# Optimization experiments

Measured on AMD Instinct MI355X. Metric: run time of the kernel, lower is better.

Reference implementation:

```python
import jax, jax.numpy as jnp
import numpy as np

E, C, F, K = 8, 768, 3072, 2  # NUM_EXPERTS, EMBED_DIM, FFN_DIM, TOP_K


def setup_inputs() -> dict:
    key = jax.random.key(0)
    k0, k1, k2, k3 = jax.random.split(key, 4)
    B, T = 8, 2048
    return {
        "x": jax.random.normal(k0, (B, T, C), jnp.float32),
        "router_w": jax.random.normal(k1, (E, C), jnp.float32) * 0.02,
        "w1": jax.random.normal(k2, (E, C, F), jnp.float32) * 0.02,
        "b1": jnp.zeros((E, F), jnp.float32),
        "w2": jax.random.normal(k3, (E, F, C), jnp.float32) * 0.02,
        "b2": jnp.zeros((E, C), jnp.float32),
    }


def reference(x, router_w, w1, b1, w2, b2):
    # Dropout is inference-mode identity (eval). GELU is torch's exact (erf) variant.
    B, T, Cc = x.shape
    flat = x.reshape(-1, Cc)                                   # [N, C]
    logits = flat @ router_w.T                                 # [N, E]
    probs = jax.nn.softmax(logits.astype(jnp.float32), axis=-1)
    top_w, top_i = jax.lax.top_k(probs, K)                     # [N, K]
    top_w = (top_w / top_w.sum(-1, keepdims=True)).astype(x.dtype)
    out = jnp.zeros_like(flat)
    for e in range(E):
        # per-token combine weight for expert e (0 if token not routed to e)
        w_e = jnp.sum(top_w * (top_i == e), axis=-1)[:, None]  # [N, 1]
        h = jax.nn.gelu(flat @ w1[e] + b1[e], approximate=False)  # [N, F]
        out = out + w_e * (h @ w2[e] + b2[e])
    return out.reshape(B, T, Cc)
```

## Files before the change

kernel.cpp:

```cpp
#include <hip/hip_runtime.h>
#include <hip/hip_bf16.h>

#define NTOK 16384
#define CDIM 768
#define FDIM 3072
#define NEXP 8
#define NSLOT 32768
#define HBLK 128
#define MAXTILES 263

typedef __attribute__((ext_vector_type(8))) short bf16x8;
typedef __attribute__((ext_vector_type(4))) float f32x4;

__device__ __forceinline__ unsigned short f2bf(float f) {
  unsigned int u = __float_as_uint(f);
  u += 0x7FFFu + ((u >> 16) & 1u);
  return (unsigned short)(u >> 16);
}
__device__ __forceinline__ float bf2f(unsigned short h) {
  return __uint_as_float((unsigned int)h << 16);
}

__device__ __forceinline__ void async16(const void* g, void* l) {
  __builtin_amdgcn_global_load_lds(
      (const __attribute__((address_space(1))) unsigned int*)g,
      (__attribute__((address_space(3))) unsigned int*)l, 16, 0, 0);
}

__global__ __launch_bounds__(256)
void k_transpose(const float* __restrict__ src, unsigned short* __restrict__ dst,
                 int R, int Cc)
{
  __shared__ float tle[32][33];
  int e = blockIdx.z;
  int c0 = blockIdx.x * 32, r0 = blockIdx.y * 32;
  int tx = threadIdx.x & 31, ty = threadIdx.x >> 5;
  const float* s = src + (size_t)e * R * Cc;
  unsigned short* d = dst + (size_t)e * R * Cc;
#pragma unroll
  for (int i = 0; i < 4; ++i)
    tle[ty + i * 8][tx] = s[(size_t)(r0 + ty + i * 8) * Cc + c0 + tx];
  __syncthreads();
#pragma unroll
  for (int i = 0; i < 4; ++i)
    d[(size_t)(c0 + ty + i * 8) * R + r0 + tx] = f2bf(tle[tx][ty + i * 8]);
}

__global__ __launch_bounds__(256)
void k_router(const float* __restrict__ x, const float* __restrict__ rw,
              int* __restrict__ tk_e, float* __restrict__ tk_w)
{
  __shared__ float srw[NEXP * CDIM];
  int tid = threadIdx.x;
#pragma unroll
  for (int i = 0; i < (NEXP * CDIM / 4) / 256; ++i)
    ((float4*)srw)[tid + i * 256] = ((const float4*)rw)[tid + i * 256];
  __syncthreads();
  int lane = tid & 63, wid = tid >> 6;
  int t = blockIdx.x * 4 + wid;
  float a[NEXP];
#pragma unroll
  for (int e = 0; e < NEXP; ++e) a[e] = 0.f;
  const float* xr = x + (size_t)t * CDIM;
#pragma unroll
  for (int c = 0; c < CDIM / 64; ++c) {
    float xv = xr[c * 64 + lane];
#pragma unroll
    for (int e = 0; e < NEXP; ++e) a[e] += xv * srw[e * CDIM + c * 64 + lane];
  }
#pragma unroll
  for (int e = 0; e < NEXP; ++e) {
#pragma unroll
    for (int off = 32; off; off >>= 1) a[e] += __shfl_xor(a[e], off);
  }
  if (lane == 0) {
    int i0 = 0; float l0 = a[0];
#pragma unroll
    for (int e = 1; e < NEXP; ++e) if (a[e] > l0) { l0 = a[e]; i0 = e; }
    int i1 = -1; float l1 = -1e30f;
#pragma unroll
    for (int e = 0; e < NEXP; ++e) if (e != i0 && a[e] > l1) { l1 = a[e]; i1 = e; }
    float w0 = 1.f / (1.f + expf(l1 - l0));
    tk_e[2 * t] = i0;     tk_e[2 * t + 1] = i1;
    tk_w[2 * t] = w0;     tk_w[2 * t + 1] = 1.f - w0;
  }
}

__global__ __launch_bounds__(256)
void k_hist(const int* __restrict__ tk_e, int* __restrict__ blockhist)
{
  __shared__ int h[NEXP];
  int tid = threadIdx.x;
  if (tid < NEXP) h[tid] = 0;
  __syncthreads();
  int e = tk_e[blockIdx.x * 256 + tid];
  atomicAdd(&h[e], 1);
  __syncthreads();
  if (tid < NEXP) blockhist[blockIdx.x * NEXP + tid] = h[tid];
}

__global__ __launch_bounds__(512)
void k_scan2(const int* __restrict__ blockhist, int* __restrict__ counts,
             int* __restrict__ offsets, int* __restrict__ tp,
             int* __restrict__ blockbase)
{
  __shared__ int ltot[NEXP];
  __shared__ int loff[NEXP + 1];
  int tid = threadIdx.x;
  int lane = tid & 63, e = tid >> 6;
  int o0 = blockhist[lane * NEXP + e];
  int o1 = blockhist[(64 + lane) * NEXP + e];
  int h0 = o0, h1 = o1;
#pragma unroll
  for (int d = 1; d < 64; d <<= 1) { int v = __shfl_up(h0, d); if (lane >= d) h0 += v; }
  int s0 = __shfl(h0, 63);
#pragma unroll
  for (int d = 1; d < 64; d <<= 1) { int v = __shfl_up(h1, d); if (lane >= d) h1 += v; }
  h1 += s0;
  if (lane == 63) ltot[e] = h1;
  __syncthreads();
  if (tid == 0) {
    loff[0] = 0;
    int tpv = 0; tp[0] = 0;
    for (int k = 0; k < NEXP; ++k) {
      loff[k + 1] = loff[k] + ltot[k];
      counts[k] = ltot[k];
      offsets[k] = loff[k];
      tpv += (ltot[k] + 127) / 128;
      tp[k + 1] = tpv;
    }
    offsets[NEXP] = loff[NEXP];
  }
  __syncthreads();
  int base = loff[e];
  blockbase[lane * NEXP + e]        = base + h0 - o0;
  blockbase[(64 + lane) * NEXP + e] = base + h1 - o1;
}

__global__ __launch_bounds__(256)
void k_assign_gather(const float* __restrict__ x, const int* __restrict__ tk_e,
                     const float* __restrict__ tk_w,
                     const int* __restrict__ blockbase,
                     int* __restrict__ tok2slot, float* __restrict__ slot_w,
                     unsigned short* __restrict__ Xg)
{
  __shared__ int eh[256];
  __shared__ int sslot[256];
  int b = blockIdx.x, tid = threadIdx.x;
  int pick = b * 256 + tid;
  int e = tk_e[pick];
  eh[tid] = e;
  __syncthreads();
  int rank = 0;
  for (int j = 0; j < tid; ++j) rank += (eh[j] == e);
  int slot = blockbase[b * NEXP + e] + rank;
  sslot[tid] = slot;
  tok2slot[pick] = slot;
  slot_w[slot] = tk_w[pick];
  __syncthreads();
  int lane = tid & 63, wid = tid >> 6;
  for (int p = wid * 64; p < wid * 64 + 64; ++p) {
    int token = (b * 256 + p) >> 1;
    int s = sslot[p];
    const float4* src = (const float4*)(x + (size_t)token * CDIM);
    ushort4* dst = (ushort4*)(Xg + (size_t)s * CDIM);
#pragma unroll
    for (int i = 0; i < 3; ++i) {
      float4 v = src[i * 64 + lane];
      ushort4 hh;
      hh.x = f2bf(v.x); hh.y = f2bf(v.y); hh.z = f2bf(v.z); hh.w = f2bf(v.w);
      dst[i * 64 + lane] = hh;
    }
  }
}

template <int EPI>
__device__ __forceinline__ void gemm_body(
    const unsigned short* __restrict__ A, int lda,
    const unsigned short* __restrict__ B, int ldb, long sB,
    int Ksteps,
    const int* __restrict__ counts, const int* __restrict__ offsets,
    const int* __restrict__ tp, int t0,
    const float* __restrict__ bias, int biasStride,
    unsigned short* __restrict__ Hout, int ldh,
    unsigned short* __restrict__ Yout, const float* __restrict__ slot_w,
    int gx, int nwg)
{
  __shared__ __align__(16) char lds[5 * 16384];

  int orig = blockIdx.y * gx + blockIdx.x;
  int q = nwg >> 3, r = nwg & 7;
  int xcd = orig & 7, j = orig >> 3;
  int wgid = (xcd < r ? xcd * (q + 1) : r * (q + 1) + (xcd - r) * q) + j;
  int bx = wgid % gx, byl = wgid / gx;
  int by = t0 + byl;

  if (by >= tp[NEXP]) return;
  int e = 0;
  while (by >= tp[e + 1]) ++e;
  int m0 = (by - tp[e]) * 128;
  int cnt = counts[e];
  int rowbase = offsets[e];
  int n0 = bx * 128;

  const unsigned short* Bexp = B + (long)e * sB + (long)n0 * ldb;
  const unsigned short* Aexp =
      (EPI == 0) ? A + (long)(rowbase + m0) * lda
                 : A + (long)(byl * 128) * lda;

  int tid = threadIdx.x;
  int lane = tid & 63, wid = tid >> 6;
  int wm = wid >> 1, wn = wid & 1;
  int ar = lane & 15, kg = lane >> 4;
  int kgs = (kg ^ ((ar >> 1) & 3)) << 4;

  int rA0 = tid >> 2;
  int cA0 = tid & 3;
  int ksw = (cA0 ^ ((rA0 >> 1) & 3)) << 3;
  const unsigned short* As0 = Aexp + (long)rA0 * lda + ksw;
  const unsigned short* As1 = Aexp + (long)(rA0 + 64) * lda + ksw;
  const unsigned short* Bs0 = Bexp + (long)rA0 * ldb + ksw;
  const unsigned short* Bs1 = Bexp + (long)(rA0 + 64) * ldb + ksw;

  f32x4 acc[4][4] = {};

  auto STAGE = [&](int t) {
    char* bb = lds + (t % 5) * 16384;
    int ko = t * 32;
    async16(As0 + ko, bb + wid * 1024);
    async16(As1 + ko, bb + 4096 + wid * 1024);
    async16(Bs0 + ko, bb + 8192 + wid * 1024);
    async16(Bs1 + ko, bb + 12288 + wid * 1024);
  };

  STAGE(0); STAGE(1); STAGE(2);

  for (int ks = 0; ks < Ksteps; ++ks) {
    if (ks + 3 < Ksteps) {
      STAGE(ks + 3);
      asm volatile("s_waitcnt vmcnt(12)" ::: "memory");
    } else if (ks + 2 < Ksteps) {
      asm volatile("s_waitcnt vmcnt(8)" ::: "memory");
    } else if (ks + 1 < Ksteps) {
      asm volatile("s_waitcnt vmcnt(4)" ::: "memory");
    } else {
      asm volatile("s_waitcnt vmcnt(0)" ::: "memory");
    }
    __builtin_amdgcn_s_barrier();
    asm volatile("" ::: "memory");

    const char* bb = lds + (ks % 5) * 16384;
    const char* bA = bb + (wm * 64 + ar) * 64 + kgs;
    const char* bB = bb + 8192 + (wn * 64 + ar) * 64 + kgs;
    bf16x8 af[4], bfr[4];
#pragma unroll
    for (int i = 0; i < 4; ++i) af[i] = *(const bf16x8*)(bA + i * 1024);
#pragma unroll
    for (int i = 0; i < 4; ++i) bfr[i] = *(const bf16x8*)(bB + i * 1024);
#pragma unroll
    for (int mi = 0; mi < 4; ++mi)
#pragma unroll
      for (int ni = 0; ni < 4; ++ni)
        acc[mi][ni] = __builtin_amdgcn_mfma_f32_16x16x32_bf16(af[mi], bfr[ni],
                                                              acc[mi][ni], 0, 0, 0);
  }

  if (EPI == 0) {
#pragma unroll
    for (int ni = 0; ni < 4; ++ni) {
      int ncol = n0 + wn * 64 + ni * 16 + ar;
      float bv = bias[e * biasStride + ncol];
#pragma unroll
      for (int mi = 0; mi < 4; ++mi) {
#pragma unroll
        for (int r = 0; r < 4; ++r) {
          int rowl = wm * 64 + mi * 16 + kg * 4 + r;
          if (m0 + rowl < cnt) {
            float v = acc[mi][ni][r] + bv;
            v = 0.5f * v * (1.0f + erff(v * 0.70710678118654752f));
            Hout[(long)(byl * 128 + rowl) * ldh + ncol] = f2bf(v);
          }
        }
      }
    }
  } else {
#pragma unroll
    for (int mi = 0; mi < 4; ++mi) {
#pragma unroll
      for (int r = 0; r < 4; ++r) {
        int rowl = wm * 64 + mi * 16 + kg * 4 + r;
        if (m0 + rowl < cnt) {
          int slot = rowbase + m0 + rowl;
          float wt = slot_w[slot];
          unsigned short* dst = Yout + (long)slot * CDIM;
#pragma unroll
          for (int ni = 0; ni < 4; ++ni) {
            int ncol = n0 + wn * 64 + ni * 16 + ar;
            float v = (acc[mi][ni][r] + bias[e * biasStride + ncol]) * wt;
            dst[ncol] = f2bf(v);
          }
        }
      }
    }
  }
}

__global__ __launch_bounds__(256)
void k_gemm1(const unsigned short* __restrict__ A, int lda,
             const unsigned short* __restrict__ B, int ldb, long sB,
             int Ksteps, const int* __restrict__ counts,
             const int* __restrict__ offsets, const int* __restrict__ tp,
             int t0, const float* __restrict__ bias, int biasStride,
             unsigned short* __restrict__ Hout, int ldh, int gx, int nwg)
{
  gemm_body<0>(A, lda, B, ldb, sB, Ksteps, counts, offsets, tp, t0,
               bias, biasStride, Hout, ldh, nullptr, nullptr, gx, nwg);
}

__global__ __launch_bounds__(256)
void k_gemm2(const unsigned short* __restrict__ A, int lda,
             const unsigned short* __restrict__ B, int ldb, long sB,
             int Ksteps, const int* __restrict__ counts,
             const int* __restrict__ offsets, const int* __restrict__ tp,
             int t0, const float* __restrict__ bias, int biasStride,
             unsigned short* __restrict__ Yout, const float* __restrict__ slot_w,
             int gx, int nwg)
{
  gemm_body<1>(A, lda, B, ldb, sB, Ksteps, counts, offsets, tp, t0,
               bias, biasStride, nullptr, 0, Yout, slot_w, gx, nwg);
}

__global__ __launch_bounds__(256)
void k_combine(const unsigned short* __restrict__ Y,
               const int* __restrict__ tok2slot, float* __restrict__ out)
{
  int t = blockIdx.x * 4 + (threadIdx.x >> 6);
  int lane = threadIdx.x & 63;
  int s0 = tok2slot[2 * t], s1 = tok2slot[2 * t + 1];
  const ushort4* y0 = (const ushort4*)(Y + (size_t)s0 * CDIM);
  const ushort4* y1 = (const ushort4*)(Y + (size_t)s1 * CDIM);
  float4* o = (float4*)(out + (size_t)t * CDIM);
#pragma unroll
  for (int i = 0; i < 3; ++i) {
    ushort4 a = y0[i * 64 + lane];
    ushort4 b = y1[i * 64 + lane];
    float4 r;
    r.x = bf2f(a.x) + bf2f(b.x);
    r.y = bf2f(a.y) + bf2f(b.y);
    r.z = bf2f(a.z) + bf2f(b.z);
    r.w = bf2f(a.w) + bf2f(b.w);
    o[i * 64 + lane] = r;
  }
}

extern "C" void kernel_launch(void* const* d_in, const int* in_sizes, int n_in,
                              void* d_out, int out_size, void* d_ws, size_t ws_size,
                              hipStream_t stream) {
  const float* x        = (const float*)d_in[0];
  const float* router_w = (const float*)d_in[1];
  const float* w1       = (const float*)d_in[2];
  const float* b1       = (const float*)d_in[3];
  const float* w2       = (const float*)d_in[4];
  const float* b2       = (const float*)d_in[5];
  float* out = (float*)d_out;

  char* ws = (char*)d_ws;
  size_t off = 0;
  auto alloc = [&](size_t bytes) -> void* {
    void* p = ws + off;
    off = (off + bytes + 255) & ~(size_t)255;
    return p;
  };
  int*   counts     = (int*)alloc(NEXP * 4);
  int*   offsets    = (int*)alloc((NEXP + 1) * 4);
  int*   tp         = (int*)alloc((NEXP + 1) * 4);
  int*   tk_e       = (int*)alloc((size_t)NSLOT * 4);
  float* tk_w       = (float*)alloc((size_t)NSLOT * 4);
  int*   blockhist  = (int*)alloc((size_t)HBLK * NEXP * 4);
  int*   blockbase  = (int*)alloc((size_t)HBLK * NEXP * 4);
  int*   tok2slot   = (int*)alloc((size_t)NSLOT * 4);
  float* slot_w     = (float*)alloc((size_t)NSLOT * 4);
  unsigned short* Yslot = (unsigned short*)alloc((size_t)NSLOT * CDIM * 2);
  unsigned short* w1t = (unsigned short*)alloc((size_t)NEXP * FDIM * CDIM * 2);
  unsigned short* w2t = (unsigned short*)alloc((size_t)NEXP * CDIM * FDIM * 2);
  unsigned short* Xg  = (unsigned short*)alloc((size_t)(NSLOT + 128) * CDIM * 2);
  int TPC = 132;
  if (off + ((size_t)TPC * 128 + 128) * FDIM * 2 > ws_size) TPC = 66;
  unsigned short* H = (unsigned short*)alloc(((size_t)TPC * 128 + 128) * FDIM * 2);

  k_transpose<<<dim3(FDIM / 32, CDIM / 32, NEXP), 256, 0, stream>>>(w1, w1t, CDIM, FDIM);
  k_transpose<<<dim3(CDIM / 32, FDIM / 32, NEXP), 256, 0, stream>>>(w2, w2t, FDIM, CDIM);
  k_router<<<NTOK / 4, 256, 0, stream>>>(x, router_w, tk_e, tk_w);
  k_hist<<<HBLK, 256, 0, stream>>>(tk_e, blockhist);
  k_scan2<<<1, 512, 0, stream>>>(blockhist, counts, offsets, tp, blockbase);
  k_assign_gather<<<HBLK, 256, 0, stream>>>(x, tk_e, tk_w, blockbase,
                                            tok2slot, slot_w, Xg);

  for (int t0 = 0; t0 < MAXTILES; t0 += TPC) {
    int yT = (MAXTILES - t0 < TPC) ? (MAXTILES - t0) : TPC;
    int gx1 = FDIM / 128;
    k_gemm1<<<dim3(gx1, yT), 256, 0, stream>>>(
        Xg, CDIM, w1t, CDIM, (long)FDIM * CDIM, CDIM / 32,
        counts, offsets, tp, t0, b1, FDIM, H, FDIM, gx1, gx1 * yT);
    int gx2 = CDIM / 128;
    k_gemm2<<<dim3(gx2, yT), 256, 0, stream>>>(
        H, FDIM, w2t, FDIM, (long)CDIM * FDIM, FDIM / 32,
        counts, offsets, tp, t0, b2, CDIM, Yslot, slot_w, gx2, gx2 * yT);
  }
  k_combine<<<NTOK / 4, 256, 0, stream>>>(Yslot, tok2slot, out);
}
```

Measured before the change: 752.2 us.

## Stage GEMM epilogues through LDS for vector stores, regroup tile order, shrink chunk

```diff
diff --git a/kernel.cpp b/kernel.cpp
--- a/kernel.cpp
+++ b/kernel.cpp
@@ -11,6 +11,7 @@
 
 typedef __attribute__((ext_vector_type(8))) short bf16x8;
 typedef __attribute__((ext_vector_type(4))) float f32x4;
+typedef __attribute__((ext_vector_type(8))) unsigned short u16x8;
 
 __device__ __forceinline__ unsigned short f2bf(float f) {
   unsigned int u = __float_as_uint(f);
@@ -190,9 +191,16 @@
 
   int orig = blockIdx.y * gx + blockIdx.x;
   int q = nwg >> 3, r = nwg & 7;
-  int xcd = orig & 7, j = orig >> 3;
-  int wgid = (xcd < r ? xcd * (q + 1) : r * (q + 1) + (xcd - r) * q) + j;
-  int bx = wgid % gx, byl = wgid / gx;
+  int xcd = orig & 7, jj = orig >> 3;
+  int wgid = (xcd < r ? xcd * (q + 1) : r * (q + 1) + (xcd - r) * q) + jj;
+  const int RG = 16;
+  int yT = nwg / gx;
+  int gsize = gx * RG;
+  int rg = wgid / gsize;
+  int rem = wgid - rg * gsize;
+  int rgs = yT - rg * RG; if (rgs > RG) rgs = RG;
+  int bx = rem / rgs;
+  int byl = rg * RG + (rem - bx * rgs);
   int by = t0 + byl;
 
   if (by >= tp[NEXP]) return;
@@ -265,42 +273,55 @@
                                                               acc[mi][ni], 0, 0, 0);
   }
 
+  unsigned short* st = (unsigned short*)lds;
+  __syncthreads();
+
   if (EPI == 0) {
 #pragma unroll
     for (int ni = 0; ni < 4; ++ni) {
-      int ncol = n0 + wn * 64 + ni * 16 + ar;
-      float bv = bias[e * biasStride + ncol];
+      int col = wn * 64 + ni * 16 + ar;
+      float bv = bias[e * biasStride + n0 + col];
 #pragma unroll
       for (int mi = 0; mi < 4; ++mi) {
 #pragma unroll
-        for (int r = 0; r < 4; ++r) {
-          int rowl = wm * 64 + mi * 16 + kg * 4 + r;
-          if (m0 + rowl < cnt) {
-            float v = acc[mi][ni][r] + bv;
-            v = 0.5f * v * (1.0f + erff(v * 0.70710678118654752f));
-            Hout[(long)(byl * 128 + rowl) * ldh + ncol] = f2bf(v);
-          }
+        for (int rr = 0; rr < 4; ++rr) {
+          int row = wm * 64 + mi * 16 + kg * 4 + rr;
+          float v = acc[mi][ni][rr] + bv;
+          v = 0.5f * v * (1.0f + erff(v * 0.70710678118654752f));
+          st[row * 136 + col] = f2bf(v);
         }
       }
     }
+    __syncthreads();
+    int row = tid >> 1, half = tid & 1;
+    unsigned short* drow = Hout + (long)(byl * 128 + row) * ldh + n0 + half * 64;
+    const unsigned short* srow = st + row * 136 + half * 64;
+#pragma unroll
+    for (int i = 0; i < 8; ++i)
+      *(u16x8*)(drow + i * 8) = *(const u16x8*)(srow + i * 8);
   } else {
 #pragma unroll
     for (int mi = 0; mi < 4; ++mi) {
 #pragma unroll
-      for (int r = 0; r < 4; ++r) {
-        int rowl = wm * 64 + mi * 16 + kg * 4 + r;
-        if (m0 + rowl < cnt) {
-          int slot = rowbase + m0 + rowl;
-          float wt = slot_w[slot];
-          unsigned short* dst = Yout + (long)slot * CDIM;
-#pragma unroll
-          for (int ni = 0; ni < 4; ++ni) {
-            int ncol = n0 + wn * 64 + ni * 16 + ar;
-            float v = (acc[mi][ni][r] + bias[e * biasStride + ncol]) * wt;
-            dst[ncol] = f2bf(v);
-          }
+      for (int rr = 0; rr < 4; ++rr) {
+        int rowl = wm * 64 + mi * 16 + kg * 4 + rr;
+        float wt = (m0 + rowl < cnt) ? slot_w[rowbase + m0 + rowl] : 0.f;
+#pragma unroll
+        for (int ni = 0; ni < 4; ++ni) {
+          int col = wn * 64 + ni * 16 + ar;
+          float v = (acc[mi][ni][rr] + bias[e * biasStride + n0 + col]) * wt;
+          st[rowl * 136 + col] = f2bf(v);
         }
       }
+    }
+    __syncthreads();
+    int row = tid >> 1, half = tid & 1;
+    if (m0 + row < cnt) {
+      unsigned short* drow = Yout + (long)(rowbase + m0 + row) * CDIM + n0 + half * 64;
+      const unsigned short* srow = st + row * 136 + half * 64;
+#pragma unroll
+      for (int i = 0; i < 8; ++i)
+        *(u16x8*)(drow + i * 8) = *(const u16x8*)(srow + i * 8);
     }
   }
 }
@@ -384,8 +405,8 @@
   unsigned short* w1t = (unsigned short*)alloc((size_t)NEXP * FDIM * CDIM * 2);
   unsigned short* w2t = (unsigned short*)alloc((size_t)NEXP * CDIM * FDIM * 2);
   unsigned short* Xg  = (unsigned short*)alloc((size_t)(NSLOT + 128) * CDIM * 2);
-  int TPC = 132;
-  if (off + ((size_t)TPC * 128 + 128) * FDIM * 2 > ws_size) TPC = 66;
+  int TPC = 66;
+  if (off + ((size_t)TPC * 128 + 128) * FDIM * 2 > ws_size) TPC = 33;
   unsigned short* H = (unsigned short*)alloc(((size_t)TPC * 128 + 128) * FDIM * 2);
 
   k_transpose<<<dim3(FDIM / 32, CDIM / 32, NEXP), 256, 0, stream>>>(w1, w1t, CDIM, FDIM);
```

Result: no change. 753.8 us (+0.2%).
